# Kernel optimization log

Hardware: AMD Instinct MI355X
Metric: run time of the kernel (lower is better)

The kernel has to match this reference:

```python
import jax, jax.numpy as jnp
import numpy as np

N = 50000        # nodes
E = 800_000      # edges (avg degree 16)
D_IN, D_HID, D_OUT = 512, 512, 256
P_DROP = 0.5


def setup_inputs() -> dict:
    key = jax.random.key(0)
    k0, k1, k2, k3 = jax.random.split(key, 4)
    x = jax.random.normal(k0, (N, D_IN), dtype=jnp.float32)
    edge_index = jax.random.randint(k1, (2, E), 0, N, dtype=jnp.int64)
    W1 = jax.random.normal(k2, (D_HID, D_IN), dtype=jnp.float32) * 0.02
    b1 = jnp.zeros((D_HID,), dtype=jnp.float32)
    W2 = jax.random.normal(k3, (D_OUT, D_HID), dtype=jnp.float32) * 0.02
    b2 = jnp.zeros((D_OUT,), dtype=jnp.float32)
    return {"x": x, "edge_index": edge_index, "W1": W1, "b1": b1, "W2": W2, "b2": b2}


def _gcn_norm(edge_index, n):
    # add self loops, then symmetric GCN normalization: D^-1/2 (A+I) D^-1/2
    src, dst = edge_index[0], edge_index[1]
    loops = jnp.arange(n, dtype=src.dtype)
    src = jnp.concatenate([src, loops])
    dst = jnp.concatenate([dst, loops])
    deg = jax.ops.segment_sum(jnp.ones_like(src, dtype=jnp.float32), dst, num_segments=n)
    dinv = jax.lax.rsqrt(deg)  # deg >= 1 because of self loops
    norm = dinv[src] * dinv[dst]  # [E+N]
    return src, dst, norm


def _propagate(x, src, dst, norm):
    # out[i] = sum_{(j->i)} norm_e * x[j]
    return jax.ops.segment_sum(x[src] * norm[:, None], dst, num_segments=x.shape[0])


def reference(x, edge_index, W1, b1, W2, b2):
    src, dst, norm = _gcn_norm(edge_index, x.shape[0])
    # SGConv layer 1 (K=1): propagate then linear
    h = _propagate(x, src, dst, norm) @ W1.T + b1
    h = jax.nn.relu(h)
    # F.dropout(p) with training=True default -> deterministic fixed-key mask here
    keep = jax.random.bernoulli(jax.random.key(42), 1.0 - P_DROP, h.shape)
    embedding = jnp.where(keep, h / (1.0 - P_DROP), 0.0)
    # SGConv layer 2
    out = _propagate(embedding, src, dst, norm) @ W2.T + b2
    return embedding, out
```

## Files before the change

kernel.cpp:

```cpp
#include <hip/hip_runtime.h>

typedef unsigned short u16t;
typedef __attribute__((ext_vector_type(8))) short short8;
typedef __attribute__((ext_vector_type(4))) short short4v;
typedef __attribute__((ext_vector_type(4))) float f32x4;
typedef __attribute__((ext_vector_type(4))) unsigned short u16x4;
typedef __attribute__((ext_vector_type(4))) unsigned int u32x4;
typedef __attribute__((ext_vector_type(4))) int i32x4;

__device__ __forceinline__ float bf2f(short b) {
  return __uint_as_float(((unsigned)(unsigned short)b) << 16);
}
__device__ __forceinline__ u16t f2bf(float f) {
  unsigned u = __float_as_uint(f);
  u += 0x7FFFu + ((u >> 16) & 1u);
  return (u16t)(u >> 16);
}

__device__ __forceinline__ bool keep_mask(unsigned flat) {
  const unsigned k0 = 0u, k1 = 42u;
  const unsigned k2 = k0 ^ k1 ^ 0x1BD11BDAu;
  unsigned x0 = 0u + k0;
  unsigned x1 = flat + k1;
#define TF_R(r) { x0 += x1; x1 = (x1 << r) | (x1 >> (32 - r)); x1 ^= x0; }
  TF_R(13) TF_R(15) TF_R(26) TF_R(6)  x0 += k1; x1 += k2 + 1u;
  TF_R(17) TF_R(29) TF_R(16) TF_R(24) x0 += k2; x1 += k0 + 2u;
  TF_R(13) TF_R(15) TF_R(26) TF_R(6)  x0 += k0; x1 += k1 + 3u;
  TF_R(17) TF_R(29) TF_R(16) TF_R(24) x0 += k1; x1 += k2 + 4u;
  TF_R(13) TF_R(15) TF_R(26) TF_R(6)  x0 += k2; x1 += k0 + 5u;
#undef TF_R
  return ((x0 ^ x1) >> 31) == 0u;
}

__device__ __forceinline__ void load_lds16(const u16t* g, u16t* l) {
  __builtin_amdgcn_global_load_lds((__attribute__((address_space(1))) void*)g,
                                   (__attribute__((address_space(3))) void*)l,
                                   16, 0, 0);
}

__global__ void cvt_bf16(const float* __restrict__ s, u16t* __restrict__ d, int n) {
  int i = (blockIdx.x * 256 + threadIdx.x) * 4;
  if (i < n) {
    f32x4 v = *(const f32x4*)&s[i];
    u16x4 o = { f2bf(v.x), f2bf(v.y), f2bf(v.z), f2bf(v.w) };
    *(u16x4*)&d[i] = o;
  }
}

__global__ __launch_bounds__(256) void cvt_x_mask(const float* __restrict__ s,
    u16t* __restrict__ d, unsigned* __restrict__ mask, int n, int nwords) {
  int t = blockIdx.x * 256 + threadIdx.x;
  int i = t * 4;
  if (i < n) {
    f32x4 v = *(const f32x4*)&s[i];
    u16x4 o = { f2bf(v.x), f2bf(v.y), f2bf(v.z), f2bf(v.w) };
    *(u16x4*)&d[i] = o;
  }
  if (t < nwords) {
    unsigned base = (unsigned)t * 32u;
    unsigned m = 0u;
    for (int k = 0; k < 32; ++k) m |= (keep_mask(base + (unsigned)k) ? 1u : 0u) << k;
    mask[t] = m;
  }
}

__global__ void count_edges(const int* __restrict__ dst, int E, int* __restrict__ cnt) {
  int e = blockIdx.x * 256 + threadIdx.x;
  if (e < E) atomicAdd(&cnt[dst[e]], 1);
}

__global__ __launch_bounds__(256) void rowp_build(const int* __restrict__ cnt,
    i32x4* __restrict__ ndr, int* __restrict__ cursor, float* __restrict__ dinv,
    int* __restrict__ gctr, u16t* __restrict__ colu, int n) {
  __shared__ int sd[256];
  __shared__ int sbase;
  const int tid = threadIdx.x;
  const int i = blockIdx.x * 256 + tid;
  int c = (i < n) ? cnt[i] : 0;
  int cs = c + 1;
  int p = (i < n) ? ((cs + 7) & ~7) : 0;
  int v = p;
  sd[tid] = v;
  __syncthreads();
  for (int o = 1; o < 256; o <<= 1) {
    int t2 = (tid >= o) ? sd[tid - o] : 0;
    __syncthreads();
    v += t2;
    sd[tid] = v;
    __syncthreads();
  }
  if (tid == 255) sbase = atomicAdd(gctr, v);
  __syncthreads();
  if (i < n) {
    int start = sbase + v - p;
    cursor[i] = start;
    float dv = rsqrtf((float)cs);
    dinv[i] = dv;
    i32x4 r;
    r[0] = start; r[1] = start + p; r[2] = __float_as_int(dv); r[3] = 0;
    ndr[i] = r;
    colu[start + c] = (u16t)i;
    for (int q = c + 1; q < p; ++q) colu[start + q] = (u16t)n;
  }
}

__global__ void fill_csr(const int* __restrict__ src, const int* __restrict__ dst, int E,
                         int* __restrict__ cursor, u16t* __restrict__ col) {
  int e = blockIdx.x * 256 + threadIdx.x;
  if (e < E) {
    int d = dst[e];
    int pos = atomicAdd(&cursor[d], 1);
    col[pos] = (u16t)src[e];
  }
}

__global__ __launch_bounds__(256) void gemm_bt_sl(const u16t* __restrict__ A,
                                                  const u16t* __restrict__ B,
                                                  u16t* __restrict__ C,
                                                  int K, int Mrows,
                                                  const float* __restrict__ dinv,
                                                  int Nclamp) {
  __shared__ __align__(16) u16t lA[128 * 32];
  __shared__ __align__(16) u16t lB[128 * 32];
  const int tid = threadIdx.x;
  const int wave = tid >> 6, lane = tid & 63;
  const int wm = (wave & 1) * 64, wn = (wave >> 1) * 64;
  const int lrow = lane & 15, lq = lane >> 4;
  const u16t* Ab = A + (size_t)blockIdx.x * 128 * K;
  const u16t* Bb = B + (size_t)blockIdx.y * 128 * K;
  const int r0 = tid >> 2, c0 = (tid & 3) * 8;
  const int ldsOff = __builtin_amdgcn_readfirstlane((tid >> 6) * 512);

  f32x4 acc[4][4];
  const f32x4 zero = {0.f, 0.f, 0.f, 0.f};
#pragma unroll
  for (int mi = 0; mi < 4; ++mi)
#pragma unroll
    for (int ni = 0; ni < 4; ++ni) acc[mi][ni] = zero;

  for (int kt = 0; kt < K; kt += 32) {
    __syncthreads();
    load_lds16(Ab + (size_t)r0 * K + kt + c0, &lA[ldsOff]);
    load_lds16(Ab + (size_t)(r0 + 64) * K + kt + c0, &lA[2048 + ldsOff]);
    load_lds16(Bb + (size_t)r0 * K + kt + c0, &lB[ldsOff]);
    load_lds16(Bb + (size_t)(r0 + 64) * K + kt + c0, &lB[2048 + ldsOff]);
    __syncthreads();
    short8 af[4], bfr[4];
#pragma unroll
    for (int mi = 0; mi < 4; ++mi)
      af[mi] = *(const short8*)&lA[(wm + mi * 16 + lrow) * 32 + lq * 8];
#pragma unroll
    for (int ni = 0; ni < 4; ++ni)
      bfr[ni] = *(const short8*)&lB[(wn + ni * 16 + lrow) * 32 + lq * 8];
#pragma unroll
    for (int mi = 0; mi < 4; ++mi)
#pragma unroll
      for (int ni = 0; ni < 4; ++ni)
        acc[mi][ni] = __builtin_amdgcn_mfma_f32_16x16x32_bf16(af[mi], bfr[ni], acc[mi][ni], 0, 0, 0);
  }

  const int crow0 = blockIdx.x * 128 + wm + lq * 4;
  const int ccol0 = blockIdx.y * 128 + wn + lrow;
#pragma unroll
  for (int mi = 0; mi < 4; ++mi)
#pragma unroll
    for (int r = 0; r < 4; ++r) {
      const int row = crow0 + mi * 16 + r;
      const float dr = (row < Nclamp) ? dinv[row] : 0.f;
#pragma unroll
      for (int ni = 0; ni < 4; ++ni) {
        int cc = ccol0 + ni * 16;
        size_t idx = ((size_t)(cc >> 5) * Mrows + row) * 32 + (cc & 31);
        C[idx] = f2bf(dr * acc[mi][ni][r]);
      }
    }
}

__device__ __forceinline__ void gather8(const u16t* __restrict__ T, u32x4 cw,
                                        float acc[4]) {
  int c[8];
#pragma unroll
  for (int q = 0; q < 4; ++q) {
    c[2 * q]     = (int)(cw[q] & 0xFFFFu);
    c[2 * q + 1] = (int)(cw[q] >> 16);
  }
  short4v u[8];
#pragma unroll
  for (int q = 0; q < 8; ++q) u[q] = *(const short4v*)&T[(size_t)c[q] * 32];
#pragma unroll
  for (int q = 0; q < 8; ++q)
#pragma unroll
    for (int j = 0; j < 4; ++j) acc[j] += bf2f(u[q][j]);
}

__global__ __launch_bounds__(256) void prop1_kernel(const u16t* __restrict__ T0,
    const u16t* __restrict__ colu, const i32x4* __restrict__ ndr,
    const float* __restrict__ b1, const unsigned* __restrict__ kmask,
    float* __restrict__ embf, u16t* __restrict__ embb, int n, int Mrows, int chunks) {
  const int t = threadIdx.x;
  const int g = (t >> 3) & 1;
  const int fl4 = (t & 7) * 4;
  const int bid = blockIdx.x;
  const int half = chunks << 3;
  const int phase = bid >= half;
  const int rem = bid - (phase ? half : 0);
  const int sl = (rem & 7) + (phase << 3);
  const int i = (rem >> 3) * 16 + (t >> 4);
  if (i >= n) return;

  const u16t* T = T0 + (size_t)sl * Mrows * 32 + fl4;
  const i32x4 nd = ndr[i];
  const float di = __int_as_float(nd[2]);
  float acc[4] = {0.f, 0.f, 0.f, 0.f};

  int e = nd[0] + g * 8;
  const int end = nd[1];
  if (e < end) {
    u32x4 cw = *(const u32x4*)&colu[e];
    e += 16;
    while (e < end) {
      u32x4 nw = *(const u32x4*)&colu[e];
      e += 16;
      gather8(T, cw, acc);
      cw = nw;
    }
    gather8(T, cw, acc);
  }

#pragma unroll
  for (int j = 0; j < 4; ++j) acc[j] += __shfl_xor(acc[j], 8, 64);

  if ((t & 15) < 8) {
    const int f = sl * 32 + fl4;
    const unsigned km = kmask[i * 16 + sl];
    f32x4 o;
    short4v ob;
#pragma unroll
    for (int j = 0; j < 4; ++j) {
      float h = di * acc[j] + b1[f + j];
      h = fmaxf(h, 0.f);
      float eb = ((km >> (fl4 + j)) & 1u) ? 2.f * h : 0.f;
      o[j] = eb;
      ob[j] = (short)f2bf(eb);
    }
    __builtin_nontemporal_store(o, (f32x4*)&embf[(size_t)i * 512 + f]);
    __builtin_nontemporal_store(ob, (short4v*)&embb[(size_t)i * 512 + f]);
  }
}

__global__ __launch_bounds__(256) void prop2_kernel(const u16t* __restrict__ T0,
    const u16t* __restrict__ colu, const i32x4* __restrict__ ndr,
    const float* __restrict__ b2, float* __restrict__ outp, int n, int Mrows) {
  const int t = threadIdx.x;
  const int g = (t >> 3) & 1;
  const int fl4 = (t & 7) * 4;
  const int bid = blockIdx.x;
  const int sl = bid & 7;
  const int i = (bid >> 3) * 16 + (t >> 4);
  if (i >= n) return;

  const u16t* T = T0 + (size_t)sl * Mrows * 32 + fl4;
  const i32x4 nd = ndr[i];
  const float di = __int_as_float(nd[2]);
  float acc[4] = {0.f, 0.f, 0.f, 0.f};

  int e = nd[0] + g * 8;
  const int end = nd[1];
  if (e < end) {
    u32x4 cw = *(const u32x4*)&colu[e];
    e += 16;
    while (e < end) {
      u32x4 nw = *(const u32x4*)&colu[e];
      e += 16;
      gather8(T, cw, acc);
      cw = nw;
    }
    gather8(T, cw, acc);
  }

#pragma unroll
  for (int j = 0; j < 4; ++j) acc[j] += __shfl_xor(acc[j], 8, 64);

  if ((t & 15) < 8) {
    const int f = sl * 32 + fl4;
    f32x4 o;
#pragma unroll
    for (int j = 0; j < 4; ++j) o[j] = di * acc[j] + b2[f + j];
    __builtin_nontemporal_store(o, (f32x4*)&outp[(size_t)i * 256 + f]);
  }
}

extern "C" void kernel_launch(void* const* d_in, const int* in_sizes, int n_in,
                              void* d_out, int out_size, void* d_ws, size_t ws_size,
                              hipStream_t stream) {
  (void)n_in; (void)out_size; (void)ws_size;
  const float* x  = (const float*)d_in[0];
  const int*   ei = (const int*)d_in[1];
  const float* W1 = (const float*)d_in[2];
  const float* b1 = (const float*)d_in[3];
  const float* W2 = (const float*)d_in[4];
  const float* b2 = (const float*)d_in[5];

  const int Nn = in_sizes[0] / 512;
  const int E  = in_sizes[1] / 2;
  const int Mpad = ((Nn + 127) / 128) * 128;
  const int K = 512;
  const int CH16 = (Nn + 15) / 16;

  char* ws = (char*)d_ws;
  size_t off = 0;
  auto take = [&](size_t bytes) -> char* {
    char* p = ws + off;
    off += (bytes + 255) & ~(size_t)255;
    return p;
  };
  u16t* xb   = (u16t*)take((size_t)Mpad * 512 * 2);
  u16t* y1s  = (u16t*)take((size_t)16 * Mpad * 32 * 2);
  u16t* W1b  = (u16t*)take((size_t)512 * 512 * 2);
  u16t* W2b  = (u16t*)take((size_t)256 * 512 * 2);
  int*   cnt    = (int*)take((size_t)(Nn + 1) * 4);
  int*   cursor = (int*)take((size_t)Nn * 4);
  float* dinv   = (float*)take((size_t)Nn * 4);
  i32x4* ndr    = (i32x4*)take((size_t)Nn * 16);
  u16t*  colu   = (u16t*)take((size_t)(E + 8 * (Nn + 1)) * 2);
  unsigned* kmask = (unsigned*)take((size_t)Nn * 16 * 4);

  float* embf = (float*)d_out;
  float* outf = (float*)d_out + (size_t)Nn * 512;

  hipMemsetAsync(cnt, 0, (size_t)(Nn + 1) * 4, stream);

  const int n1 = Nn * 512;
  cvt_x_mask<<<(n1 / 4 + 255) / 256, 256, 0, stream>>>(x, xb, kmask, n1, Nn * 16);
  cvt_bf16<<<(512 * 512 / 4 + 255) / 256, 256, 0, stream>>>(W1, W1b, 512 * 512);
  cvt_bf16<<<(256 * 512 / 4 + 255) / 256, 256, 0, stream>>>(W2, W2b, 256 * 512);

  count_edges<<<(E + 255) / 256, 256, 0, stream>>>(ei + E, E, cnt);
  rowp_build<<<(Nn + 255) / 256, 256, 0, stream>>>(cnt, ndr, cursor, dinv, cnt + Nn,
                                                   colu, Nn);
  fill_csr<<<(E + 255) / 256, 256, 0, stream>>>(ei, ei + E, E, cursor, colu);

  dim3 g1(Mpad / 128, 4);
  gemm_bt_sl<<<g1, 256, 0, stream>>>(xb, W1b, y1s, K, Mpad, dinv, Nn);
  prop1_kernel<<<16 * CH16, 256, 0, stream>>>(y1s, colu, ndr, b1, kmask,
                                              embf, xb , Nn, Mpad, CH16);

  u16t* zs = y1s;
  dim3 g2(Mpad / 128, 2);
  gemm_bt_sl<<<g2, 256, 0, stream>>>(xb, W2b, zs, K, Mpad, dinv, Nn);
  prop2_kernel<<<8 * CH16, 256, 0, stream>>>(zs, colu, ndr, b2, outf, Nn, Mpad);
}
```

Measured before the change: 623.9 us.

## Bin nodes by degree and assign one node per 8 lanes in propagation

Adds a degree histogram and a bucketed permutation so the propagation kernels process nodes grouped by similar padded degree, which cuts warp divergence from uneven row lengths. Each node now uses 8 lanes instead of 16 split into two halves, so the cross-half shuffle reduction goes away. The gather uses byte offsets with packed bf16 unpacking into float2 accumulators. The dropout mask is stored transposed so reads are coalesced per slice. In exchange it adds two small kernels, atomics in rowp_build, and output writes that scatter because they follow the permuted node order.

```diff
diff --git a/kernel.cpp b/kernel.cpp
--- a/kernel.cpp
+++ b/kernel.cpp
@@ -4,8 +4,10 @@
 typedef __attribute__((ext_vector_type(8))) short short8;
 typedef __attribute__((ext_vector_type(4))) short short4v;
 typedef __attribute__((ext_vector_type(4))) float f32x4;
+typedef __attribute__((ext_vector_type(2))) float f32x2;
 typedef __attribute__((ext_vector_type(4))) unsigned short u16x4;
 typedef __attribute__((ext_vector_type(4))) unsigned int u32x4;
+typedef __attribute__((ext_vector_type(2))) unsigned int u32x2;
 typedef __attribute__((ext_vector_type(4))) int i32x4;
 
 __device__ __forceinline__ float bf2f(short b) {
@@ -48,7 +50,7 @@
 }
 
 __global__ __launch_bounds__(256) void cvt_x_mask(const float* __restrict__ s,
-    u16t* __restrict__ d, unsigned* __restrict__ mask, int n, int nwords) {
+    u16t* __restrict__ d, unsigned* __restrict__ mask, int n, int nn) {
   int t = blockIdx.x * 256 + threadIdx.x;
   int i = t * 4;
   if (i < n) {
@@ -56,11 +58,11 @@
     u16x4 o = { f2bf(v.x), f2bf(v.y), f2bf(v.z), f2bf(v.w) };
     *(u16x4*)&d[i] = o;
   }
-  if (t < nwords) {
+  if (t < nn * 16) {
     unsigned base = (unsigned)t * 32u;
     unsigned m = 0u;
     for (int k = 0; k < 32; ++k) m |= (keep_mask(base + (unsigned)k) ? 1u : 0u) << k;
-    mask[t] = m;
+    mask[(size_t)(t & 15) * nn + (t >> 4)] = m;
   }
 }
 
@@ -69,9 +71,25 @@
   if (e < E) atomicAdd(&cnt[dst[e]], 1);
 }
 
+__global__ void bin_hist(const int* __restrict__ cnt, int* __restrict__ hist, int n) {
+  int i = blockIdx.x * 256 + threadIdx.x;
+  if (i < n) {
+    int b = (cnt[i] + 8) >> 3;
+    atomicAdd(&hist[b < 15 ? b : 15], 1);
+  }
+}
+
+__global__ void bin_scan(const int* __restrict__ hist, int* __restrict__ binCursor) {
+  if (threadIdx.x == 0 && blockIdx.x == 0) {
+    int s = 0;
+    for (int b = 0; b < 16; ++b) { binCursor[b] = s; s += hist[b]; }
+  }
+}
+
 __global__ __launch_bounds__(256) void rowp_build(const int* __restrict__ cnt,
     i32x4* __restrict__ ndr, int* __restrict__ cursor, float* __restrict__ dinv,
-    int* __restrict__ gctr, u16t* __restrict__ colu, int n) {
+    int* __restrict__ gctr, u16t* __restrict__ colu,
+    int* __restrict__ binCursor, u16t* __restrict__ perm, int n) {
   __shared__ int sd[256];
   __shared__ int sbase;
   const int tid = threadIdx.x;
@@ -101,6 +119,10 @@
     ndr[i] = r;
     colu[start + c] = (u16t)i;
     for (int q = c + 1; q < p; ++q) colu[start + q] = (u16t)n;
+    int b = p >> 3;
+    b = b < 15 ? b : 15;
+    int slot = atomicAdd(&binCursor[b], 1);
+    perm[slot] = (u16t)i;
   }
 }
 
@@ -176,118 +198,113 @@
     }
 }
 
-__device__ __forceinline__ void gather8(const u16t* __restrict__ T, u32x4 cw,
-                                        float acc[4]) {
-  int c[8];
+__device__ __forceinline__ void gather8(const char* __restrict__ Tb, u32x4 cw,
+                                        unsigned flb, f32x2& a01, f32x2& a23) {
+  unsigned off[8];
 #pragma unroll
   for (int q = 0; q < 4; ++q) {
-    c[2 * q]     = (int)(cw[q] & 0xFFFFu);
-    c[2 * q + 1] = (int)(cw[q] >> 16);
-  }
-  short4v u[8];
-#pragma unroll
-  for (int q = 0; q < 8; ++q) u[q] = *(const short4v*)&T[(size_t)c[q] * 32];
-#pragma unroll
-  for (int q = 0; q < 8; ++q)
-#pragma unroll
-    for (int j = 0; j < 4; ++j) acc[j] += bf2f(u[q][j]);
+    off[2 * q]     = ((cw[q] & 0xFFFFu) << 6) | flb;
+    off[2 * q + 1] = ((cw[q] >> 16) << 6) | flb;
+  }
+  u32x2 w[8];
+#pragma unroll
+  for (int q = 0; q < 8; ++q) w[q] = *(const u32x2*)(Tb + (size_t)off[q]);
+#pragma unroll
+  for (int q = 0; q < 8; ++q) {
+    f32x2 v01 = { __uint_as_float(w[q].x << 16), __uint_as_float(w[q].x & 0xFFFF0000u) };
+    f32x2 v23 = { __uint_as_float(w[q].y << 16), __uint_as_float(w[q].y & 0xFFFF0000u) };
+    a01 += v01;
+    a23 += v23;
+  }
 }
 
 __global__ __launch_bounds__(256) void prop1_kernel(const u16t* __restrict__ T0,
     const u16t* __restrict__ colu, const i32x4* __restrict__ ndr,
-    const float* __restrict__ b1, const unsigned* __restrict__ kmask,
+    const u16t* __restrict__ perm, const float* __restrict__ b1,
+    const unsigned* __restrict__ kmask,
     float* __restrict__ embf, u16t* __restrict__ embb, int n, int Mrows, int chunks) {
   const int t = threadIdx.x;
-  const int g = (t >> 3) & 1;
+  const unsigned flb = (unsigned)(t & 7) * 8u;
   const int fl4 = (t & 7) * 4;
   const int bid = blockIdx.x;
   const int half = chunks << 3;
   const int phase = bid >= half;
   const int rem = bid - (phase ? half : 0);
   const int sl = (rem & 7) + (phase << 3);
-  const int i = (rem >> 3) * 16 + (t >> 4);
-  if (i >= n) return;
-
-  const u16t* T = T0 + (size_t)sl * Mrows * 32 + fl4;
+  const int slot = (rem >> 3) * 32 + (t >> 3);
+  if (slot >= n) return;
+  const int i = (int)perm[slot];
+
+  const char* Tb = (const char*)T0 + (size_t)sl * ((size_t)Mrows * 64);
   const i32x4 nd = ndr[i];
   const float di = __int_as_float(nd[2]);
-  float acc[4] = {0.f, 0.f, 0.f, 0.f};
-
-  int e = nd[0] + g * 8;
+  f32x2 a01 = {0.f, 0.f}, a23 = {0.f, 0.f};
+
+  int e = nd[0];
   const int end = nd[1];
-  if (e < end) {
-    u32x4 cw = *(const u32x4*)&colu[e];
-    e += 16;
-    while (e < end) {
-      u32x4 nw = *(const u32x4*)&colu[e];
-      e += 16;
-      gather8(T, cw, acc);
-      cw = nw;
-    }
-    gather8(T, cw, acc);
-  }
-
-#pragma unroll
-  for (int j = 0; j < 4; ++j) acc[j] += __shfl_xor(acc[j], 8, 64);
-
-  if ((t & 15) < 8) {
-    const int f = sl * 32 + fl4;
-    const unsigned km = kmask[i * 16 + sl];
-    f32x4 o;
-    short4v ob;
-#pragma unroll
-    for (int j = 0; j < 4; ++j) {
-      float h = di * acc[j] + b1[f + j];
-      h = fmaxf(h, 0.f);
-      float eb = ((km >> (fl4 + j)) & 1u) ? 2.f * h : 0.f;
-      o[j] = eb;
-      ob[j] = (short)f2bf(eb);
-    }
-    __builtin_nontemporal_store(o, (f32x4*)&embf[(size_t)i * 512 + f]);
-    __builtin_nontemporal_store(ob, (short4v*)&embb[(size_t)i * 512 + f]);
-  }
+  u32x4 cw = *(const u32x4*)&colu[e];
+  e += 8;
+  while (e < end) {
+    u32x4 nw = *(const u32x4*)&colu[e];
+    e += 8;
+    gather8(Tb, cw, flb, a01, a23);
+    cw = nw;
+  }
+  gather8(Tb, cw, flb, a01, a23);
+
+  const int f = sl * 32 + fl4;
+  const unsigned km = kmask[(size_t)sl * n + i];
+  float acc[4] = {a01.x, a01.y, a23.x, a23.y};
+  f32x4 o;
+  short4v ob;
+#pragma unroll
+  for (int j = 0; j < 4; ++j) {
+    float h = di * acc[j] + b1[f + j];
+    h = fmaxf(h, 0.f);
+    float eb = ((km >> (fl4 + j)) & 1u) ? 2.f * h : 0.f;
+    o[j] = eb;
+    ob[j] = (short)f2bf(eb);
+  }
+  __builtin_nontemporal_store(o, (f32x4*)&embf[(size_t)i * 512 + f]);
+  __builtin_nontemporal_store(ob, (short4v*)&embb[(size_t)i * 512 + f]);
 }
 
 __global__ __launch_bounds__(256) void prop2_kernel(const u16t* __restrict__ T0,
     const u16t* __restrict__ colu, const i32x4* __restrict__ ndr,
-    const float* __restrict__ b2, float* __restrict__ outp, int n, int Mrows) {
+    const u16t* __restrict__ perm, const float* __restrict__ b2,
+    float* __restrict__ outp, int n, int Mrows) {
   const int t = threadIdx.x;
-  const int g = (t >> 3) & 1;
+  const unsigned flb = (unsigned)(t & 7) * 8u;
   const int fl4 = (t & 7) * 4;
   const int bid = blockIdx.x;
   const int sl = bid & 7;
-  const int i = (bid >> 3) * 16 + (t >> 4);
-  if (i >= n) return;
-
-  const u16t* T = T0 + (size_t)sl * Mrows * 32 + fl4;
+  const int slot = (bid >> 3) * 32 + (t >> 3);
+  if (slot >= n) return;
+  const int i = (int)perm[slot];
+
+  const char* Tb = (const char*)T0 + (size_t)sl * ((size_t)Mrows * 64);
   const i32x4 nd = ndr[i];
   const float di = __int_as_float(nd[2]);
-  float acc[4] = {0.f, 0.f, 0.f, 0.f};
-
-  int e = nd[0] + g * 8;
+  f32x2 a01 = {0.f, 0.f}, a23 = {0.f, 0.f};
+
+  int e = nd[0];
   const int end = nd[1];
-  if (e < end) {
-    u32x4 cw = *(const u32x4*)&colu[e];
-    e += 16;
-    while (e < end) {
-      u32x4 nw = *(const u32x4*)&colu[e];
-      e += 16;
-      gather8(T, cw, acc);
-      cw = nw;
-    }
-    gather8(T, cw, acc);
-  }
-
-#pragma unroll
-  for (int j = 0; j < 4; ++j) acc[j] += __shfl_xor(acc[j], 8, 64);
-
-  if ((t & 15) < 8) {
-    const int f = sl * 32 + fl4;
-    f32x4 o;
-#pragma unroll
-    for (int j = 0; j < 4; ++j) o[j] = di * acc[j] + b2[f + j];
-    __builtin_nontemporal_store(o, (f32x4*)&outp[(size_t)i * 256 + f]);
-  }
+  u32x4 cw = *(const u32x4*)&colu[e];
+  e += 8;
+  while (e < end) {
+    u32x4 nw = *(const u32x4*)&colu[e];
+    e += 8;
+    gather8(Tb, cw, flb, a01, a23);
+    cw = nw;
+  }
+  gather8(Tb, cw, flb, a01, a23);
+
+  const int f = sl * 32 + fl4;
+  float acc[4] = {a01.x, a01.y, a23.x, a23.y};
+  f32x4 o;
+#pragma unroll
+  for (int j = 0; j < 4; ++j) o[j] = di * acc[j] + b2[f + j];
+  __builtin_nontemporal_store(o, (f32x4*)&outp[(size_t)i * 256 + f]);
 }
 
 extern "C" void kernel_launch(void* const* d_in, const int* in_sizes, int n_in,
@@ -305,7 +322,7 @@
   const int E  = in_sizes[1] / 2;
   const int Mpad = ((Nn + 127) / 128) * 128;
   const int K = 512;
-  const int CH16 = (Nn + 15) / 16;
+  const int CH = (Nn + 31) / 32;
 
   char* ws = (char*)d_ws;
   size_t off = 0;
@@ -318,35 +335,42 @@
   u16t* y1s  = (u16t*)take((size_t)16 * Mpad * 32 * 2);
   u16t* W1b  = (u16t*)take((size_t)512 * 512 * 2);
   u16t* W2b  = (u16t*)take((size_t)256 * 512 * 2);
-  int*   cnt    = (int*)take((size_t)(Nn + 1) * 4);
+  int*   cnt    = (int*)take((size_t)(Nn + 33) * 4);
   int*   cursor = (int*)take((size_t)Nn * 4);
   float* dinv   = (float*)take((size_t)Nn * 4);
   i32x4* ndr    = (i32x4*)take((size_t)Nn * 16);
-  u16t*  colu   = (u16t*)take((size_t)(E + 8 * (Nn + 1)) * 2);
+  u16t*  perm   = (u16t*)take((size_t)Nn * 2);
+  u16t*  colu   = (u16t*)take((size_t)(E + 8 * (Nn + 1) + 64) * 2);
   unsigned* kmask = (unsigned*)take((size_t)Nn * 16 * 4);
 
   float* embf = (float*)d_out;
   float* outf = (float*)d_out + (size_t)Nn * 512;
 
-  hipMemsetAsync(cnt, 0, (size_t)(Nn + 1) * 4, stream);
+  int* gctr      = cnt + Nn;
+  int* hist      = cnt + Nn + 1;
+  int* binCursor = cnt + Nn + 17;
+
+  hipMemsetAsync(cnt, 0, (size_t)(Nn + 33) * 4, stream);
 
   const int n1 = Nn * 512;
-  cvt_x_mask<<<(n1 / 4 + 255) / 256, 256, 0, stream>>>(x, xb, kmask, n1, Nn * 16);
+  cvt_x_mask<<<(n1 / 4 + 255) / 256, 256, 0, stream>>>(x, xb, kmask, n1, Nn);
   cvt_bf16<<<(512 * 512 / 4 + 255) / 256, 256, 0, stream>>>(W1, W1b, 512 * 512);
   cvt_bf16<<<(256 * 512 / 4 + 255) / 256, 256, 0, stream>>>(W2, W2b, 256 * 512);
 
   count_edges<<<(E + 255) / 256, 256, 0, stream>>>(ei + E, E, cnt);
-  rowp_build<<<(Nn + 255) / 256, 256, 0, stream>>>(cnt, ndr, cursor, dinv, cnt + Nn,
-                                                   colu, Nn);
+  bin_hist<<<(Nn + 255) / 256, 256, 0, stream>>>(cnt, hist, Nn);
+  bin_scan<<<1, 64, 0, stream>>>(hist, binCursor);
+  rowp_build<<<(Nn + 255) / 256, 256, 0, stream>>>(cnt, ndr, cursor, dinv, gctr,
+                                                   colu, binCursor, perm, Nn);
   fill_csr<<<(E + 255) / 256, 256, 0, stream>>>(ei, ei + E, E, cursor, colu);
 
   dim3 g1(Mpad / 128, 4);
   gemm_bt_sl<<<g1, 256, 0, stream>>>(xb, W1b, y1s, K, Mpad, dinv, Nn);
-  prop1_kernel<<<16 * CH16, 256, 0, stream>>>(y1s, colu, ndr, b1, kmask,
-                                              embf, xb , Nn, Mpad, CH16);
+  prop1_kernel<<<16 * CH, 256, 0, stream>>>(y1s, colu, ndr, perm, b1, kmask,
+                                            embf, xb , Nn, Mpad, CH);
 
   u16t* zs = y1s;
   dim3 g2(Mpad / 128, 2);
   gemm_bt_sl<<<g2, 256, 0, stream>>>(xb, W2b, zs, K, Mpad, dinv, Nn);
-  prop2_kernel<<<8 * CH16, 256, 0, stream>>>(zs, colu, ndr, b2, outf, Nn, Mpad);
-}
+  prop2_kernel<<<8 * CH, 256, 0, stream>>>(zs, colu, ndr, perm, b2, outf, Nn, Mpad);
+}
```

Result: slower. 1.342 ms (+115.0%).
